# Optimization experiments

Measured on AMD Instinct MI355X. Metric: run time of the kernel, lower is better.

## Reference

```python
import jax, jax.numpy as jnp
import numpy as np
import math

B, T, C = 2, 2048, 2048
NH = 16
HS = C // NH

def setup_inputs() -> dict:
    key = jax.random.key(0)
    k1, k2, k3 = jax.random.split(key, 3)
    x = jax.random.normal(k1, (B, T, C), dtype=jnp.float32)
    w_attn = jax.random.normal(k2, (3 * C, C), dtype=jnp.float32) * 0.02
    w_proj = jax.random.normal(k3, (C, C), dtype=jnp.float32) * 0.02
    return {"x": x, "w_attn": w_attn, "w_proj": w_proj}

def reference(x, w_attn, w_proj):
    Bx, Tx, Cx = x.shape
    # qkv projection: Linear(C, 3C), no bias
    qkv = jnp.einsum('btc,oc->bto', x, w_attn)  # [B,T,3C]
    q, k, v = jnp.split(qkv, 3, axis=-1)
    # reshape to heads: [B,T,H,hs]
    q = q.reshape(Bx, Tx, NH, HS)
    k = k.reshape(Bx, Tx, NH, HS)
    v = v.reshape(Bx, Tx, NH, HS)
    # scores [B,H,Tq,Tk]
    att = jnp.einsum('bqhd,bkhd->bhqk', q, k) * (1.0 / math.sqrt(HS))
    causal = jnp.tril(jnp.ones((Tx, Tx), dtype=bool))
    att = jnp.where(causal[None, None], att, -jnp.inf)
    att = jax.nn.softmax(att, axis=-1)
    # attn_dropout with p=0.0 is identity
    y = jnp.einsum('bhqk,bkhd->bqhd', att, v)
    y = y.reshape(Bx, Tx, Cx)
    return jnp.einsum('btc,oc->bto', y, w_proj)
```

## Files before the change

kernel.cpp:

```cpp
#include <hip/hip_runtime.h>

typedef __attribute__((ext_vector_type(8))) short short8;
typedef __attribute__((ext_vector_type(4))) float f32x4;
typedef unsigned short u16;

#define T_SEQ 2048
#define C_DIM 2048

static __device__ __forceinline__ u16 f2bf(float f){
  unsigned u = __float_as_uint(f);
  u = (u + 0x7fffu + ((u >> 16) & 1u)) >> 16;
  return (u16)u;
}

__global__ void cvt3_kernel(const float* __restrict__ x,
                            const float* __restrict__ wa,
                            const float* __restrict__ wp,
                            u16* __restrict__ xb, u16* __restrict__ wab,
                            u16* __restrict__ wpb){
  int idx = blockIdx.x * blockDim.x + threadIdx.x;
  int stride = gridDim.x * blockDim.x;
  for (int i = idx; i < 6291456; i += stride){
    const float* src; u16* dst; int j;
    if (i < 2097152){ src = x;  dst = xb;  j = i; }
    else if (i < 5242880){ src = wa; dst = wab; j = i - 2097152; }
    else { src = wp; dst = wpb; j = i - 5242880; }
    float4 v = ((const float4*)src)[j];
    ushort4 o;
    o.x = f2bf(v.x); o.y = f2bf(v.y); o.z = f2bf(v.z); o.w = f2bf(v.w);
    ((ushort4*)dst)[j] = o;
  }
}

__device__ __forceinline__ void gl_lds16(const void* g, void* l){
  __builtin_amdgcn_global_load_lds(
      (const __attribute__((address_space(1))) unsigned int*)g,
      (__attribute__((address_space(3))) unsigned int*)l,
      16, 0, 0);
}

template<int MODE, typename OUT>
__global__ __launch_bounds__(256, 2) void gemm256(const u16* __restrict__ A,
                                                  const u16* __restrict__ B,
                                                  OUT* __restrict__ C,
                                                  u16* __restrict__ VT,
                                                  int M, int N, int K){
  __shared__ __align__(16) u16 lA[2][128*64];
  __shared__ __align__(16) u16 lB[2][128*64];
  const int tid  = threadIdx.x;
  const int lane = tid & 63;
  const int r16  = lane & 15;
  const int g4   = lane >> 4;
  const int wave = tid >> 6;
  const int wm = wave >> 1, wn = wave & 1;

  const int nwg = gridDim.x * gridDim.y;
  const int idl = blockIdx.y * gridDim.x + blockIdx.x;
  const int wg  = (idl & 7) * (nwg >> 3) + (idl >> 3);
  const int bx  = wg / gridDim.y, by = wg % gridDim.y;
  const int m0 = by * 128, n0 = bx * 128;

  f32x4 acc[4][4] = {};
  const int nt = K >> 6;

  auto stA = [&](int b, int t){
    #pragma unroll
    for (int c=0;c<4;c++){
      const int row0 = wave*32 + c*8;
      const int row  = row0 + (lane>>3);
      const int cole = (((lane&7) ^ (row&7)) << 3);
      gl_lds16(&A[(size_t)(m0+row)*K + t*64 + cole], &lA[b][row0*64]);
    }
  };
  auto stB2 = [&](int b, int t, int half){
    #pragma unroll
    for (int c=0;c<2;c++){
      const int row0 = (wave>>1)*64 + half*32 + (wave&1)*16 + c*8;
      const int row  = row0 + (lane>>3);
      const int cole = (((lane&7) ^ (row&7)) << 3);
      gl_lds16(&B[(size_t)(n0+row)*K + t*64 + cole], &lB[b][row0*64]);
    }
  };
  auto rdA = [&](short8 (&af)[4][2], int b){
    #pragma unroll
    for (int i=0;i<4;i++){
      const int R = wm*64 + i*16 + r16;
      #pragma unroll
      for (int ks=0;ks<2;ks++)
        af[i][ks] = *(const short8*)&lA[b][R*64 + ((g4*8 + ks*32) ^ ((R&7)<<3))];
    }
  };
  auto rdB = [&](short8 (&bf)[2][2], int b, int half){
    #pragma unroll
    for (int j=0;j<2;j++){
      const int R = wn*64 + half*32 + j*16 + r16;
      #pragma unroll
      for (int ks=0;ks<2;ks++)
        bf[j][ks] = *(const short8*)&lB[b][R*64 + ((g4*8 + ks*32) ^ ((R&7)<<3))];
    }
  };

  stA(0,0); stB2(0,0,0); stB2(0,0,1);
  asm volatile("s_waitcnt vmcnt(2)" ::: "memory");
  __builtin_amdgcn_s_barrier();
  asm volatile("" ::: "memory");

  for (int t = 0; t < nt; ++t){
    const int cb = t & 1, nb = cb ^ 1;
    const bool more = (t + 1 < nt);
    short8 af[4][2], bf[2][2];

    rdA(af, cb); rdB(bf, cb, 0);
    if (more){
      stA(nb, t+1); stB2(nb, t+1, 0);
      asm volatile("s_waitcnt vmcnt(6)" ::: "memory");
    } else {
      asm volatile("s_waitcnt vmcnt(0)" ::: "memory");
    }
    __builtin_amdgcn_s_barrier();
    asm volatile("s_waitcnt lgkmcnt(0)" ::: "memory");
    __builtin_amdgcn_sched_barrier(0);
    __builtin_amdgcn_s_setprio(1);
    #pragma unroll
    for (int i=0;i<4;i++)
      #pragma unroll
      for (int j=0;j<2;j++)
        #pragma unroll
        for (int ks=0;ks<2;ks++)
          acc[i][j] = __builtin_amdgcn_mfma_f32_16x16x32_bf16(af[i][ks], bf[j][ks], acc[i][j], 0,0,0);
    __builtin_amdgcn_s_setprio(0);
    __builtin_amdgcn_s_barrier();
    asm volatile("" ::: "memory");

    rdB(bf, cb, 1);
    if (more){
      stB2(nb, t+1, 1);
      asm volatile("s_waitcnt vmcnt(2)" ::: "memory");
    }
    __builtin_amdgcn_s_barrier();
    asm volatile("s_waitcnt lgkmcnt(0)" ::: "memory");
    __builtin_amdgcn_sched_barrier(0);
    __builtin_amdgcn_s_setprio(1);
    #pragma unroll
    for (int i=0;i<4;i++)
      #pragma unroll
      for (int j=0;j<2;j++)
        #pragma unroll
        for (int ks=0;ks<2;ks++)
          acc[i][2+j] = __builtin_amdgcn_mfma_f32_16x16x32_bf16(af[i][ks], bf[j][ks], acc[i][2+j], 0,0,0);
    __builtin_amdgcn_s_setprio(0);
    __builtin_amdgcn_s_barrier();
    asm volatile("" ::: "memory");
  }

  if (MODE == 1 && n0 >= 4096){
    #pragma unroll
    for (int i=0;i<4;i++){
      const int m = m0 + wm*64 + i*16 + g4*4;
      const int bb = m >> 11, tt = m & 2047;
      #pragma unroll
      for (int j=0;j<4;j++){
        const int cv = n0 + wn*64 + j*16 + r16 - 4096;
        const int h = cv >> 7, dl = cv & 127;
        ushort4 pack;
        pack.x = f2bf(acc[i][j][0]); pack.y = f2bf(acc[i][j][1]);
        pack.z = f2bf(acc[i][j][2]); pack.w = f2bf(acc[i][j][3]);
        *(ushort4*)&VT[(size_t)((bb<<4) + h)*262144 + (size_t)dl*2048 + tt] = pack;
      }
    }
  } else {
    const int ldc = (MODE == 1) ? 4096 : N;
    #pragma unroll
    for (int i=0;i<4;i++){
      const int row = m0 + wm*64 + i*16 + g4*4;
      #pragma unroll
      for (int j=0;j<4;j++){
        const int col = n0 + wn*64 + j*16 + r16;
        #pragma unroll
        for (int r=0;r<4;r++){
          float v = acc[i][j][r];
          if constexpr (sizeof(OUT)==2) C[(size_t)(row+r)*ldc + col] = (OUT)f2bf(v);
          else                          C[(size_t)(row+r)*ldc + col] = (OUT)v;
        }
      }
    }
  }
}

__global__ __launch_bounds__(256) void attn_kernel(const u16* __restrict__ qk,
                                                   const u16* __restrict__ vt,
                                                   u16* __restrict__ y){
  __shared__ __align__(16) u16 Kl[2][64*128];
  __shared__ __align__(16) u16 Vl[2][128*64];
  __shared__ __align__(16) u16 Pl[4][32*64];

  const int tid = threadIdx.x, lane = tid & 63, wave = tid >> 6;
  const int r16 = lane & 15, g4 = lane >> 4;

  const int id = blockIdx.x;
  const int xk = id & 7,  kk = id >> 3;
  const int bh = 4*xk + (kk & 3);
  const int v5 = kk >> 2;
  const int qt = (v5 < 8) ? v5 : (23 - v5);

  const int b = bh >> 4, h = bh & 15;
  const int qcol = h*128, kcol = 2048 + h*128;
  const u16* vhead = vt + (size_t)bh * 262144;
  const float scale = 0.08838834764831845f;

  short8 qf[2][4];
  #pragma unroll
  for (int i=0;i<2;i++){
    const u16* qp = qk + (size_t)(b*T_SEQ + qt*128 + wave*32 + i*16 + r16)*4096 + qcol;
    #pragma unroll
    for (int c=0;c<4;c++) qf[i][c] = *(const short8*)&qp[g4*8 + c*32];
  }

  float mrow[2][4], lrow[2][4];
  #pragma unroll
  for (int i=0;i<2;i++)
    #pragma unroll
    for (int r=0;r<4;r++){ mrow[i][r] = -1e30f; lrow[i][r] = 0.f; }
  f32x4 o[2][8] = {};

  const int nt = 2*qt + 2;

  auto stage = [&](int sbuf, int t){
    const size_t kbase = (size_t)(b*T_SEQ + t*64)*4096 + kcol;
    #pragma unroll
    for (int c=0;c<4;c++){
      const int row0 = wave*16 + c*4;
      const int row  = row0 + g4;
      gl_lds16(&qk[kbase + (size_t)row*4096 + ((r16*8) ^ ((row&7)<<3))],
               &Kl[sbuf][row0*128]);
    }
    const int t0 = t*64;
    #pragma unroll
    for (int c=0;c<4;c++){
      const int idx = wave*4 + c;
      const int d   = idx*8 + (lane>>3);
      const int j8  = (lane&7)*8;
      gl_lds16(&vhead[(size_t)d*2048 + t0 + (j8 ^ ((d&7)<<3))],
               &Vl[sbuf][idx*512]);
    }
  };

  stage(0, 0);
  int cur = 0;

  for (int t = 0; t < nt; ++t){
    __syncthreads();
    if (t + 1 < nt) stage(cur^1, t+1);

    float smat[2][4][4];
    #pragma unroll
    for (int cc=0;cc<4;cc++){
      const int krow = cc*16 + r16;
      const int sw = (krow & 7) << 3;
      short8 kf[4];
      #pragma unroll
      for (int dc=0;dc<4;dc++)
        kf[dc] = *(const short8*)&Kl[cur][krow*128 + ((g4*8 + dc*32) ^ sw)];
      #pragma unroll
      for (int i=0;i<2;i++){
        f32x4 sv = {0.f,0.f,0.f,0.f};
        #pragma unroll
        for (int dc=0;dc<4;dc++)
          sv = __builtin_amdgcn_mfma_f32_16x16x32_bf16(qf[i][dc], kf[dc], sv, 0,0,0);
        #pragma unroll
        for (int rr=0;rr<4;rr++) smat[i][cc][rr] = sv[rr] * scale;
      }
    }
    if (t >= 2*qt){
      #pragma unroll
      for (int cc=0;cc<4;cc++){
        const int kvl = (t - 2*qt)*64 + cc*16 + r16;
        #pragma unroll
        for (int i=0;i<2;i++)
          #pragma unroll
          for (int rr=0;rr<4;rr++){
            const int qi = wave*32 + i*16 + g4*4 + rr;
            if (kvl > qi) smat[i][cc][rr] = -1e30f;
          }
      }
    }

    float pm[2][4];
    #pragma unroll
    for (int i=0;i<2;i++)
      #pragma unroll
      for (int rr=0;rr<4;rr++){
        float p0 = fmaxf(fmaxf(smat[i][0][rr], smat[i][1][rr]),
                         fmaxf(smat[i][2][rr], smat[i][3][rr]));
        #pragma unroll
        for (int off=1; off<16; off<<=1) p0 = fmaxf(p0, __shfl_xor(p0, off, 64));
        pm[i][rr] = p0;
      }
    bool need = false;
    #pragma unroll
    for (int i=0;i<2;i++)
      #pragma unroll
      for (int rr=0;rr<4;rr++) need = need || (pm[i][rr] > mrow[i][rr] + 8.f);
    if (__any(need)){
      #pragma unroll
      for (int i=0;i<2;i++)
        #pragma unroll
        for (int rr=0;rr<4;rr++){
          const float mnew = fmaxf(mrow[i][rr], pm[i][rr]);
          const float corr = __expf(mrow[i][rr] - mnew);
          mrow[i][rr] = mnew;
          lrow[i][rr] *= corr;
          #pragma unroll
          for (int n=0;n<8;n++) o[i][n][rr] *= corr;
        }
    }
    #pragma unroll
    for (int i=0;i<2;i++)
      #pragma unroll
      for (int rr=0;rr<4;rr++){
        float s0 = 0.f;
        #pragma unroll
        for (int cc=0;cc<4;cc++){
          const float p = __expf(smat[i][cc][rr] - mrow[i][rr]);
          smat[i][cc][rr] = p;
          s0 += p;
        }
        #pragma unroll
        for (int off=1; off<16; off<<=1) s0 += __shfl_xor(s0, off, 64);
        lrow[i][rr] += s0;
      }

    #pragma unroll
    for (int i=0;i<2;i++)
      #pragma unroll
      for (int cc=0;cc<4;cc++)
        #pragma unroll
        for (int rr=0;rr<4;rr++){
          const int qr = i*16 + g4*4 + rr;
          Pl[wave][qr*64 + ((cc*16 + r16) ^ ((qr&7)<<3))] = f2bf(smat[i][cc][rr]);
        }
    asm volatile("s_waitcnt lgkmcnt(0)" ::: "memory");

    short8 pf[2][2];
    #pragma unroll
    for (int i=0;i<2;i++){
      const int qr = i*16 + r16;
      const int sw = (qr & 7) << 3;
      pf[i][0] = *(const short8*)&Pl[wave][qr*64 + ((g4*8)      ^ sw)];
      pf[i][1] = *(const short8*)&Pl[wave][qr*64 + ((g4*8 + 32) ^ sw)];
    }
    #pragma unroll
    for (int n=0;n<8;n++){
      const int vr = n*16 + r16;
      const int sw = (vr & 7) << 3;
      short8 vf0 = *(const short8*)&Vl[cur][vr*64 + ((g4*8)      ^ sw)];
      short8 vf1 = *(const short8*)&Vl[cur][vr*64 + ((g4*8 + 32) ^ sw)];
      #pragma unroll
      for (int i=0;i<2;i++){
        o[i][n] = __builtin_amdgcn_mfma_f32_16x16x32_bf16(pf[i][0], vf0, o[i][n], 0,0,0);
        o[i][n] = __builtin_amdgcn_mfma_f32_16x16x32_bf16(pf[i][1], vf1, o[i][n], 0,0,0);
      }
    }
    cur ^= 1;
  }

  #pragma unroll
  for (int i=0;i<2;i++){
    const size_t yr0 = (size_t)(b*T_SEQ + qt*128 + wave*32 + i*16 + g4*4) * C_DIM + h*128;
    #pragma unroll
    for (int n=0;n<8;n++)
      #pragma unroll
      for (int rr=0;rr<4;rr++){
        const float v = o[i][n][rr] / lrow[i][rr];
        y[yr0 + (size_t)rr*C_DIM + n*16 + r16] = f2bf(v);
      }
  }
}

extern "C" void kernel_launch(void* const* d_in, const int* in_sizes, int n_in,
                              void* d_out, int out_size, void* d_ws, size_t ws_size,
                              hipStream_t stream){
  const float* x  = (const float*)d_in[0];
  const float* wa = (const float*)d_in[1];
  const float* wp = (const float*)d_in[2];
  float* out = (float*)d_out;

  u16* ws  = (u16*)d_ws;
  u16* xb  = ws;
  u16* wab = xb  + 8388608;
  u16* wpb = wab + 12582912;
  u16* qk  = wpb + 4194304;
  u16* vt  = qk  + 16777216;
  u16* yb  = xb;

  hipLaunchKernelGGL(cvt3_kernel, dim3(2048), dim3(256), 0, stream,
                     x, wa, wp, xb, wab, wpb);

  hipLaunchKernelGGL((gemm256<1,u16>),   dim3(48,32), dim3(256), 0, stream,
                     xb, wab, qk, vt, 4096, 6144, 2048);
  hipLaunchKernelGGL(attn_kernel,        dim3(512),  dim3(256), 0, stream,
                     qk, vt, yb);
  hipLaunchKernelGGL((gemm256<0,float>), dim3(16,32), dim3(256), 0, stream,
                     yb, wpb, out, (u16*)nullptr, 4096, 2048, 2048);
}
```

Before: 286.0 us.

## Pair complementary 64-row query tiles per block to balance causal attention work

```diff
diff --git a/kernel.cpp b/kernel.cpp
--- a/kernel.cpp
+++ b/kernel.cpp
@@ -200,18 +200,20 @@
   const int id = blockIdx.x;
   const int xk = id & 7,  kk = id >> 3;
   const int bh = 4*xk + (kk & 3);
-  const int v5 = kk >> 2;
-  const int qt = (v5 < 8) ? v5 : (23 - v5);
-
-  const int b = bh >> 4, h = bh & 15;
+  const int a  = kk >> 2;
+  const int bq = 31 - a;
+
+  const int bb = bh >> 4, h = bh & 15;
   const int qcol = h*128, kcol = 2048 + h*128;
   const u16* vhead = vt + (size_t)bh * 262144;
   const float scale = 0.08838834764831845f;
 
+  const int qbase[2] = { a*64, bq*64 };
+
   short8 qf[2][4];
   #pragma unroll
   for (int i=0;i<2;i++){
-    const u16* qp = qk + (size_t)(b*T_SEQ + qt*128 + wave*32 + i*16 + r16)*4096 + qcol;
+    const u16* qp = qk + (size_t)(bb*T_SEQ + qbase[i] + wave*16 + r16)*4096 + qcol;
     #pragma unroll
     for (int c=0;c<4;c++) qf[i][c] = *(const short8*)&qp[g4*8 + c*32];
   }
@@ -223,10 +225,10 @@
     for (int r=0;r<4;r++){ mrow[i][r] = -1e30f; lrow[i][r] = 0.f; }
   f32x4 o[2][8] = {};
 
-  const int nt = 2*qt + 2;
+  const int nt = bq + 1;
 
   auto stage = [&](int sbuf, int t){
-    const size_t kbase = (size_t)(b*T_SEQ + t*64)*4096 + kcol;
+    const size_t kbase = (size_t)(bb*T_SEQ + t*64)*4096 + kcol;
     #pragma unroll
     for (int c=0;c<4;c++){
       const int row0 = wave*16 + c*4;
@@ -251,6 +253,7 @@
   for (int t = 0; t < nt; ++t){
     __syncthreads();
     if (t + 1 < nt) stage(cur^1, t+1);
+    const bool act0 = (t <= a);
 
     float smat[2][4][4];
     #pragma unroll
@@ -261,52 +264,71 @@
       #pragma unroll
       for (int dc=0;dc<4;dc++)
         kf[dc] = *(const short8*)&Kl[cur][krow*128 + ((g4*8 + dc*32) ^ sw)];
-      #pragma unroll
-      for (int i=0;i<2;i++){
+      {
         f32x4 sv = {0.f,0.f,0.f,0.f};
         #pragma unroll
         for (int dc=0;dc<4;dc++)
-          sv = __builtin_amdgcn_mfma_f32_16x16x32_bf16(qf[i][dc], kf[dc], sv, 0,0,0);
-        #pragma unroll
-        for (int rr=0;rr<4;rr++) smat[i][cc][rr] = sv[rr] * scale;
-      }
-    }
-    if (t >= 2*qt){
+          sv = __builtin_amdgcn_mfma_f32_16x16x32_bf16(qf[1][dc], kf[dc], sv, 0,0,0);
+        #pragma unroll
+        for (int rr=0;rr<4;rr++) smat[1][cc][rr] = sv[rr] * scale;
+      }
+      if (act0){
+        f32x4 sv = {0.f,0.f,0.f,0.f};
+        #pragma unroll
+        for (int dc=0;dc<4;dc++)
+          sv = __builtin_amdgcn_mfma_f32_16x16x32_bf16(qf[0][dc], kf[dc], sv, 0,0,0);
+        #pragma unroll
+        for (int rr=0;rr<4;rr++) smat[0][cc][rr] = sv[rr] * scale;
+      }
+    }
+    if (t == a){
       #pragma unroll
       for (int cc=0;cc<4;cc++){
-        const int kvl = (t - 2*qt)*64 + cc*16 + r16;
-        #pragma unroll
-        for (int i=0;i<2;i++)
+        const int kvl = cc*16 + r16;
+        #pragma unroll
+        for (int rr=0;rr<4;rr++){
+          const int qi = wave*16 + g4*4 + rr;
+          if (kvl > qi) smat[0][cc][rr] = -1e30f;
+        }
+      }
+    }
+    if (t == bq){
+      #pragma unroll
+      for (int cc=0;cc<4;cc++){
+        const int kvl = cc*16 + r16;
+        #pragma unroll
+        for (int rr=0;rr<4;rr++){
+          const int qi = wave*16 + g4*4 + rr;
+          if (kvl > qi) smat[1][cc][rr] = -1e30f;
+        }
+      }
+    }
+
+    float lm[2][4];
+    #pragma unroll
+    for (int rr=0;rr<4;rr++)
+      lm[1][rr] = fmaxf(fmaxf(smat[1][0][rr], smat[1][1][rr]),
+                        fmaxf(smat[1][2][rr], smat[1][3][rr]));
+    if (act0)
+      #pragma unroll
+      for (int rr=0;rr<4;rr++)
+        lm[0][rr] = fmaxf(fmaxf(smat[0][0][rr], smat[0][1][rr]),
+                          fmaxf(smat[0][2][rr], smat[0][3][rr]));
+    bool need = false;
+    #pragma unroll
+    for (int rr=0;rr<4;rr++) need = need || (lm[1][rr] > mrow[1][rr] + 8.f);
+    if (act0)
+      #pragma unroll
+      for (int rr=0;rr<4;rr++) need = need || (lm[0][rr] > mrow[0][rr] + 8.f);
+    if (__any(need)){
+      const int ihi = act0 ? 0 : 1;
+      for (int i=1;i>=ihi;--i)
+        #pragma unroll
+        for (int rr=0;rr<4;rr++){
+          float pmv = lm[i][rr];
           #pragma unroll
-          for (int rr=0;rr<4;rr++){
-            const int qi = wave*32 + i*16 + g4*4 + rr;
-            if (kvl > qi) smat[i][cc][rr] = -1e30f;
-          }
-      }
-    }
-
-    float pm[2][4];
-    #pragma unroll
-    for (int i=0;i<2;i++)
-      #pragma unroll
-      for (int rr=0;rr<4;rr++){
-        float p0 = fmaxf(fmaxf(smat[i][0][rr], smat[i][1][rr]),
-                         fmaxf(smat[i][2][rr], smat[i][3][rr]));
-        #pragma unroll
-        for (int off=1; off<16; off<<=1) p0 = fmaxf(p0, __shfl_xor(p0, off, 64));
-        pm[i][rr] = p0;
-      }
-    bool need = false;
-    #pragma unroll
-    for (int i=0;i<2;i++)
-      #pragma unroll
-      for (int rr=0;rr<4;rr++) need = need || (pm[i][rr] > mrow[i][rr] + 8.f);
-    if (__any(need)){
-      #pragma unroll
-      for (int i=0;i<2;i++)
-        #pragma unroll
-        for (int rr=0;rr<4;rr++){
-          const float mnew = fmaxf(mrow[i][rr], pm[i][rr]);
+          for (int off=1; off<16; off<<=1) pmv = fmaxf(pmv, __shfl_xor(pmv, off, 64));
+          const float mnew = fmaxf(mrow[i][rr], pmv);
           const float corr = __expf(mrow[i][rr] - mnew);
           mrow[i][rr] = mnew;
           lrow[i][rr] *= corr;
@@ -314,40 +336,49 @@
           for (int n=0;n<8;n++) o[i][n][rr] *= corr;
         }
     }
-    #pragma unroll
-    for (int i=0;i<2;i++)
-      #pragma unroll
-      for (int rr=0;rr<4;rr++){
-        float s0 = 0.f;
-        #pragma unroll
-        for (int cc=0;cc<4;cc++){
-          const float p = __expf(smat[i][cc][rr] - mrow[i][rr]);
-          smat[i][cc][rr] = p;
-          s0 += p;
+    {
+      const int ihi = act0 ? 0 : 1;
+      for (int i=1;i>=ihi;--i)
+        #pragma unroll
+        for (int rr=0;rr<4;rr++){
+          float s0 = 0.f;
+          #pragma unroll
+          for (int cc=0;cc<4;cc++){
+            const float p = __expf(smat[i][cc][rr] - mrow[i][rr]);
+            smat[i][cc][rr] = p;
+            s0 += p;
+          }
+          #pragma unroll
+          for (int off=1; off<16; off<<=1) s0 += __shfl_xor(s0, off, 64);
+          lrow[i][rr] += s0;
         }
-        #pragma unroll
-        for (int off=1; off<16; off<<=1) s0 += __shfl_xor(s0, off, 64);
-        lrow[i][rr] += s0;
-      }
-
-    #pragma unroll
-    for (int i=0;i<2;i++)
-      #pragma unroll
-      for (int cc=0;cc<4;cc++)
-        #pragma unroll
-        for (int rr=0;rr<4;rr++){
-          const int qr = i*16 + g4*4 + rr;
-          Pl[wave][qr*64 + ((cc*16 + r16) ^ ((qr&7)<<3))] = f2bf(smat[i][cc][rr]);
-        }
+    }
+
+    {
+      const int ihi = act0 ? 0 : 1;
+      for (int i=1;i>=ihi;--i)
+        #pragma unroll
+        for (int cc=0;cc<4;cc++)
+          #pragma unroll
+          for (int rr=0;rr<4;rr++){
+            const int qr = i*16 + g4*4 + rr;
+            Pl[wave][qr*64 + ((cc*16 + r16) ^ ((qr&7)<<3))] = f2bf(smat[i][cc][rr]);
+          }
+    }
     asm volatile("s_waitcnt lgkmcnt(0)" ::: "memory");
 
     short8 pf[2][2];
-    #pragma unroll
-    for (int i=0;i<2;i++){
-      const int qr = i*16 + r16;
-      const int sw = (qr & 7) << 3;
-      pf[i][0] = *(const short8*)&Pl[wave][qr*64 + ((g4*8)      ^ sw)];
-      pf[i][1] = *(const short8*)&Pl[wave][qr*64 + ((g4*8 + 32) ^ sw)];
+    {
+      const int qr1 = 16 + r16;
+      const int sw1 = (qr1 & 7) << 3;
+      pf[1][0] = *(const short8*)&Pl[wave][qr1*64 + ((g4*8)      ^ sw1)];
+      pf[1][1] = *(const short8*)&Pl[wave][qr1*64 + ((g4*8 + 32) ^ sw1)];
+      if (act0){
+        const int qr0 = r16;
+        const int sw0 = (qr0 & 7) << 3;
+        pf[0][0] = *(const short8*)&Pl[wave][qr0*64 + ((g4*8)      ^ sw0)];
+        pf[0][1] = *(const short8*)&Pl[wave][qr0*64 + ((g4*8 + 32) ^ sw0)];
+      }
     }
     #pragma unroll
     for (int n=0;n<8;n++){
@@ -355,10 +386,11 @@
       const int sw = (vr & 7) << 3;
       short8 vf0 = *(const short8*)&Vl[cur][vr*64 + ((g4*8)      ^ sw)];
       short8 vf1 = *(const short8*)&Vl[cur][vr*64 + ((g4*8 + 32) ^ sw)];
-      #pragma unroll
-      for (int i=0;i<2;i++){
-        o[i][n] = __builtin_amdgcn_mfma_f32_16x16x32_bf16(pf[i][0], vf0, o[i][n], 0,0,0);
-        o[i][n] = __builtin_amdgcn_mfma_f32_16x16x32_bf16(pf[i][1], vf1, o[i][n], 0,0,0);
+      o[1][n] = __builtin_amdgcn_mfma_f32_16x16x32_bf16(pf[1][0], vf0, o[1][n], 0,0,0);
+      o[1][n] = __builtin_amdgcn_mfma_f32_16x16x32_bf16(pf[1][1], vf1, o[1][n], 0,0,0);
+      if (act0){
+        o[0][n] = __builtin_amdgcn_mfma_f32_16x16x32_bf16(pf[0][0], vf0, o[0][n], 0,0,0);
+        o[0][n] = __builtin_amdgcn_mfma_f32_16x16x32_bf16(pf[0][1], vf1, o[0][n], 0,0,0);
       }
     }
     cur ^= 1;
@@ -366,7 +398,7 @@
 
   #pragma unroll
   for (int i=0;i<2;i++){
-    const size_t yr0 = (size_t)(b*T_SEQ + qt*128 + wave*32 + i*16 + g4*4) * C_DIM + h*128;
+    const size_t yr0 = (size_t)(bb*T_SEQ + qbase[i] + wave*16 + g4*4) * C_DIM + h*128;
     #pragma unroll
     for (int n=0;n<8;n++)
       #pragma unroll
```

New measurement: 397.8 us. +39.1%, slower.

## Split attention query tile across eight waves with one 16-row slice each

Applied to the files above, without the earlier changes.

```diff
diff --git a/kernel.cpp b/kernel.cpp
--- a/kernel.cpp
+++ b/kernel.cpp
@@ -187,12 +187,12 @@
   }
 }
 
-__global__ __launch_bounds__(256) void attn_kernel(const u16* __restrict__ qk,
+__global__ __launch_bounds__(512) void attn_kernel(const u16* __restrict__ qk,
                                                    const u16* __restrict__ vt,
                                                    u16* __restrict__ y){
   __shared__ __align__(16) u16 Kl[2][64*128];
   __shared__ __align__(16) u16 Vl[2][128*64];
-  __shared__ __align__(16) u16 Pl[4][32*64];
+  __shared__ __align__(16) u16 Pl[8][16*64];
 
   const int tid = threadIdx.x, lane = tid & 63, wave = tid >> 6;
   const int r16 = lane & 15, g4 = lane >> 4;
@@ -203,41 +203,38 @@
   const int v5 = kk >> 2;
   const int qt = (v5 < 8) ? v5 : (23 - v5);
 
-  const int b = bh >> 4, h = bh & 15;
+  const int bb = bh >> 4, h = bh & 15;
   const int qcol = h*128, kcol = 2048 + h*128;
   const u16* vhead = vt + (size_t)bh * 262144;
   const float scale = 0.08838834764831845f;
 
-  short8 qf[2][4];
+  short8 qf[4];
+  {
+    const u16* qp = qk + (size_t)(bb*T_SEQ + qt*128 + wave*16 + r16)*4096 + qcol;
+    #pragma unroll
+    for (int c=0;c<4;c++) qf[c] = *(const short8*)&qp[g4*8 + c*32];
+  }
+
+  float mrow[4], lrow[4];
   #pragma unroll
-  for (int i=0;i<2;i++){
-    const u16* qp = qk + (size_t)(b*T_SEQ + qt*128 + wave*32 + i*16 + r16)*4096 + qcol;
-    #pragma unroll
-    for (int c=0;c<4;c++) qf[i][c] = *(const short8*)&qp[g4*8 + c*32];
-  }
-
-  float mrow[2][4], lrow[2][4];
-  #pragma unroll
-  for (int i=0;i<2;i++)
-    #pragma unroll
-    for (int r=0;r<4;r++){ mrow[i][r] = -1e30f; lrow[i][r] = 0.f; }
-  f32x4 o[2][8] = {};
+  for (int r=0;r<4;r++){ mrow[r] = -1e30f; lrow[r] = 0.f; }
+  f32x4 o[8] = {};
 
   const int nt = 2*qt + 2;
 
   auto stage = [&](int sbuf, int t){
-    const size_t kbase = (size_t)(b*T_SEQ + t*64)*4096 + kcol;
-    #pragma unroll
-    for (int c=0;c<4;c++){
-      const int row0 = wave*16 + c*4;
+    const size_t kbase = (size_t)(bb*T_SEQ + t*64)*4096 + kcol;
+    #pragma unroll
+    for (int c=0;c<2;c++){
+      const int row0 = wave*8 + c*4;
       const int row  = row0 + g4;
       gl_lds16(&qk[kbase + (size_t)row*4096 + ((r16*8) ^ ((row&7)<<3))],
                &Kl[sbuf][row0*128]);
     }
     const int t0 = t*64;
     #pragma unroll
-    for (int c=0;c<4;c++){
-      const int idx = wave*4 + c;
+    for (int c=0;c<2;c++){
+      const int idx = wave*2 + c;
       const int d   = idx*8 + (lane>>3);
       const int j8  = (lane&7)*8;
       gl_lds16(&vhead[(size_t)d*2048 + t0 + (j8 ^ ((d&7)<<3))],
@@ -252,7 +249,7 @@
     __syncthreads();
     if (t + 1 < nt) stage(cur^1, t+1);
 
-    float smat[2][4][4];
+    float smat[4][4];
     #pragma unroll
     for (int cc=0;cc<4;cc++){
       const int krow = cc*16 + r16;
@@ -261,93 +258,75 @@
       #pragma unroll
       for (int dc=0;dc<4;dc++)
         kf[dc] = *(const short8*)&Kl[cur][krow*128 + ((g4*8 + dc*32) ^ sw)];
-      #pragma unroll
-      for (int i=0;i<2;i++){
-        f32x4 sv = {0.f,0.f,0.f,0.f};
-        #pragma unroll
-        for (int dc=0;dc<4;dc++)
-          sv = __builtin_amdgcn_mfma_f32_16x16x32_bf16(qf[i][dc], kf[dc], sv, 0,0,0);
-        #pragma unroll
-        for (int rr=0;rr<4;rr++) smat[i][cc][rr] = sv[rr] * scale;
-      }
+      f32x4 sv = {0.f,0.f,0.f,0.f};
+      #pragma unroll
+      for (int dc=0;dc<4;dc++)
+        sv = __builtin_amdgcn_mfma_f32_16x16x32_bf16(qf[dc], kf[dc], sv, 0,0,0);
+      #pragma unroll
+      for (int rr=0;rr<4;rr++) smat[cc][rr] = sv[rr] * scale;
     }
     if (t >= 2*qt){
       #pragma unroll
       for (int cc=0;cc<4;cc++){
         const int kvl = (t - 2*qt)*64 + cc*16 + r16;
         #pragma unroll
-        for (int i=0;i<2;i++)
-          #pragma unroll
-          for (int rr=0;rr<4;rr++){
-            const int qi = wave*32 + i*16 + g4*4 + rr;
-            if (kvl > qi) smat[i][cc][rr] = -1e30f;
-          }
-      }
-    }
-
-    float pm[2][4];
-    #pragma unroll
-    for (int i=0;i<2;i++)
+        for (int rr=0;rr<4;rr++){
+          const int qi = wave*16 + g4*4 + rr;
+          if (kvl > qi) smat[cc][rr] = -1e30f;
+        }
+      }
+    }
+
+    float lm[4];
+    #pragma unroll
+    for (int rr=0;rr<4;rr++)
+      lm[rr] = fmaxf(fmaxf(smat[0][rr], smat[1][rr]), fmaxf(smat[2][rr], smat[3][rr]));
+    bool need = false;
+    #pragma unroll
+    for (int rr=0;rr<4;rr++) need = need || (lm[rr] > mrow[rr] + 8.f);
+    if (__any(need)){
       #pragma unroll
       for (int rr=0;rr<4;rr++){
-        float p0 = fmaxf(fmaxf(smat[i][0][rr], smat[i][1][rr]),
-                         fmaxf(smat[i][2][rr], smat[i][3][rr]));
-        #pragma unroll
-        for (int off=1; off<16; off<<=1) p0 = fmaxf(p0, __shfl_xor(p0, off, 64));
-        pm[i][rr] = p0;
-      }
-    bool need = false;
-    #pragma unroll
-    for (int i=0;i<2;i++)
-      #pragma unroll
-      for (int rr=0;rr<4;rr++) need = need || (pm[i][rr] > mrow[i][rr] + 8.f);
-    if (__any(need)){
-      #pragma unroll
-      for (int i=0;i<2;i++)
-        #pragma unroll
-        for (int rr=0;rr<4;rr++){
-          const float mnew = fmaxf(mrow[i][rr], pm[i][rr]);
-          const float corr = __expf(mrow[i][rr] - mnew);
-          mrow[i][rr] = mnew;
-          lrow[i][rr] *= corr;
-          #pragma unroll
-          for (int n=0;n<8;n++) o[i][n][rr] *= corr;
-        }
-    }
-    #pragma unroll
-    for (int i=0;i<2;i++)
+        float pmv = lm[rr];
+        #pragma unroll
+        for (int off=1; off<16; off<<=1) pmv = fmaxf(pmv, __shfl_xor(pmv, off, 64));
+        const float mnew = fmaxf(mrow[rr], pmv);
+        const float corr = __expf(mrow[rr] - mnew);
+        mrow[rr] = mnew;
+        lrow[rr] *= corr;
+        #pragma unroll
+        for (int n=0;n<8;n++) o[n][rr] *= corr;
+      }
+    }
+    #pragma unroll
+    for (int rr=0;rr<4;rr++){
+      float s0 = 0.f;
+      #pragma unroll
+      for (int cc=0;cc<4;cc++){
+        const float p = __expf(smat[cc][rr] - mrow[rr]);
+        smat[cc][rr] = p;
+        s0 += p;
+      }
+      #pragma unroll
+      for (int off=1; off<16; off<<=1) s0 += __shfl_xor(s0, off, 64);
+      lrow[rr] += s0;
+    }
+
+    #pragma unroll
+    for (int cc=0;cc<4;cc++)
       #pragma unroll
       for (int rr=0;rr<4;rr++){
-        float s0 = 0.f;
-        #pragma unroll
-        for (int cc=0;cc<4;cc++){
-          const float p = __expf(smat[i][cc][rr] - mrow[i][rr]);
-          smat[i][cc][rr] = p;
-          s0 += p;
-        }
-        #pragma unroll
-        for (int off=1; off<16; off<<=1) s0 += __shfl_xor(s0, off, 64);
-        lrow[i][rr] += s0;
-      }
-
-    #pragma unroll
-    for (int i=0;i<2;i++)
-      #pragma unroll
-      for (int cc=0;cc<4;cc++)
-        #pragma unroll
-        for (int rr=0;rr<4;rr++){
-          const int qr = i*16 + g4*4 + rr;
-          Pl[wave][qr*64 + ((cc*16 + r16) ^ ((qr&7)<<3))] = f2bf(smat[i][cc][rr]);
-        }
+        const int qr = g4*4 + rr;
+        Pl[wave][qr*64 + ((cc*16 + r16) ^ ((qr&7)<<3))] = f2bf(smat[cc][rr]);
+      }
     asm volatile("s_waitcnt lgkmcnt(0)" ::: "memory");
 
-    short8 pf[2][2];
-    #pragma unroll
-    for (int i=0;i<2;i++){
-      const int qr = i*16 + r16;
+    short8 pf0, pf1;
+    {
+      const int qr = r16;
       const int sw = (qr & 7) << 3;
-      pf[i][0] = *(const short8*)&Pl[wave][qr*64 + ((g4*8)      ^ sw)];
-      pf[i][1] = *(const short8*)&Pl[wave][qr*64 + ((g4*8 + 32) ^ sw)];
+      pf0 = *(const short8*)&Pl[wave][qr*64 + ((g4*8)      ^ sw)];
+      pf1 = *(const short8*)&Pl[wave][qr*64 + ((g4*8 + 32) ^ sw)];
     }
     #pragma unroll
     for (int n=0;n<8;n++){
@@ -355,23 +334,19 @@
       const int sw = (vr & 7) << 3;
       short8 vf0 = *(const short8*)&Vl[cur][vr*64 + ((g4*8)      ^ sw)];
       short8 vf1 = *(const short8*)&Vl[cur][vr*64 + ((g4*8 + 32) ^ sw)];
-      #pragma unroll
-      for (int i=0;i<2;i++){
-        o[i][n] = __builtin_amdgcn_mfma_f32_16x16x32_bf16(pf[i][0], vf0, o[i][n], 0,0,0);
-        o[i][n] = __builtin_amdgcn_mfma_f32_16x16x32_bf16(pf[i][1], vf1, o[i][n], 0,0,0);
-      }
+      o[n] = __builtin_amdgcn_mfma_f32_16x16x32_bf16(pf0, vf0, o[n], 0,0,0);
+      o[n] = __builtin_amdgcn_mfma_f32_16x16x32_bf16(pf1, vf1, o[n], 0,0,0);
     }
     cur ^= 1;
   }
 
-  #pragma unroll
-  for (int i=0;i<2;i++){
-    const size_t yr0 = (size_t)(b*T_SEQ + qt*128 + wave*32 + i*16 + g4*4) * C_DIM + h*128;
+  {
+    const size_t yr0 = (size_t)(bb*T_SEQ + qt*128 + wave*16 + g4*4) * C_DIM + h*128;
     #pragma unroll
     for (int n=0;n<8;n++)
       #pragma unroll
       for (int rr=0;rr<4;rr++){
-        const float v = o[i][n][rr] / lrow[i][rr];
+        const float v = o[n][rr] / lrow[rr];
         y[yr0 + (size_t)rr*C_DIM + n*16 + r16] = f2bf(v);
       }
   }
@@ -398,8 +373,8 @@
 
   hipLaunchKernelGGL((gemm256<1,u16>),   dim3(48,32), dim3(256), 0, stream,
                      xb, wab, qk, vt, 4096, 6144, 2048);
-  hipLaunchKernelGGL(attn_kernel,        dim3(512),  dim3(256), 0, stream,
+  hipLaunchKernelGGL(attn_kernel,        dim3(512),  dim3(512), 0, stream,
                      qk, vt, yb);
-  hipLaunchKernelGGL((gemm256<0,float>), dim3(16,32), dim3(256), 0, stream,
+  hipLaunchKernelGGL((gemm256<0,float>), dim3(16,32), dim3(512 / 2), 0, stream,
                      yb, wpb, out, (u16*)nullptr, 4096, 2048, 2048);
 }
```

Measured after the change: 254.2 us. -11.1%, faster.
